# Kernel tuning notes

Hardware: AMD Instinct MI355X
Metric: run time of the kernel (lower is better)

## Reference

```python
import jax, jax.numpy as jnp
import numpy as np

BATCH, SEQ, D_MODEL, N_HEADS, D_HEAD = 2, 2048, 2048, 16, 128
ATTN_SCALE = np.sqrt(D_HEAD).astype(np.float32)
IGNORE = jnp.float32(-1e5)


def setup_inputs() -> dict:
    key = jax.random.key(0)
    ks = jax.random.split(key, 5)
    init = 1.0 / np.sqrt(D_MODEL)
    return {
        "x": jax.random.normal(ks[0], (BATCH, SEQ, D_MODEL), jnp.float32),
        "W_Q": jax.random.normal(ks[1], (N_HEADS, D_MODEL, D_HEAD), jnp.float32) * init,
        "W_K": jax.random.normal(ks[2], (N_HEADS, D_MODEL, D_HEAD), jnp.float32) * init,
        "W_V": jax.random.normal(ks[3], (N_HEADS, D_MODEL, D_HEAD), jnp.float32) * init,
        "W_O": jax.random.normal(ks[4], (N_HEADS, D_HEAD, D_MODEL), jnp.float32) * init,
        "b_Q": jnp.zeros((N_HEADS, D_HEAD), jnp.float32),
        "b_K": jnp.zeros((N_HEADS, D_HEAD), jnp.float32),
        "b_V": jnp.zeros((N_HEADS, D_HEAD), jnp.float32),
        "b_O": jnp.zeros((D_MODEL,), jnp.float32),
    }


def reference(x, W_Q, W_K, W_V, W_O, b_Q, b_K, b_V, b_O):
    # q,k,v: [batch, pos, head, d_head]
    q = jnp.einsum('bpd,hde->bphe', x, W_Q) + b_Q
    k = jnp.einsum('bpd,hde->bphe', x, W_K) + b_K
    v = jnp.einsum('bpd,hde->bphe', x, W_V) + b_V
    # scores: [batch, head, query_pos, key_pos]
    scores = jnp.einsum('bqhe,bkhe->bhqk', q, k) / ATTN_SCALE
    S = x.shape[1]
    causal = jnp.tril(jnp.ones((S, S), bool))
    scores = jnp.where(causal, scores, IGNORE)
    attn = jax.nn.softmax(scores, axis=-1)
    z = jnp.einsum('bkhe,bhqk->bqhe', v, attn)
    out = jnp.einsum('bqhe,hed->bqd', z, W_O) + b_O
    return out
```

## Files before the change

### kernel.cpp

```cpp
#include <hip/hip_runtime.h>

typedef unsigned int uint;
typedef unsigned short ushort;
typedef __bf16 bf16x8 __attribute__((ext_vector_type(8)));
typedef float f32x4 __attribute__((ext_vector_type(4)));
typedef uint u32x4 __attribute__((ext_vector_type(4)));

#define DEV static __device__ __forceinline__

#define BATCH 2
#define SEQ 2048
#define DMODEL 2048
#define NHEADS 16
#define DHEAD 128
#define MROWS (BATCH*SEQ)
#define RSCALE 0.08838834764831845f
#define LOG2E  1.4426950408889634f

DEV float fast_exp2(float x) { return __builtin_amdgcn_exp2f(x); }

DEV bf16x8 as_frag(u32x4 v) { return __builtin_bit_cast(bf16x8, v); }
DEV ushort f2bf(float f) {
  uint u = __builtin_bit_cast(uint, f);
  u += 0x7fffu + ((u >> 16) & 1u);
  return (ushort)(u >> 16);
}
DEV u32x4 lds_ld16(const ushort* p) { return *(const u32x4*)p; }

DEV void async_cp16(const ushort* g, ushort* l) {
  __builtin_amdgcn_global_load_lds(
      (const __attribute__((address_space(1))) uint*)g,
      (__attribute__((address_space(3))) uint*)l, 16, 0, 0);
}

__global__ __launch_bounds__(256) void prep(
    const float* __restrict__ x,
    const float* __restrict__ Wq, const float* __restrict__ Wk,
    const float* __restrict__ Wv, const float* __restrict__ Wo,
    ushort* __restrict__ xb, ushort* __restrict__ WqT,
    ushort* __restrict__ WkT, ushort* __restrict__ WvT,
    ushort* __restrict__ WoT)
{
  int id = blockIdx.x;
  if (id < 8192) {
    int i = id * 256 + threadIdx.x;
    float4 v = ((const float4*)x)[i];
    union { ushort u[4]; uint2 w; } o;
    o.u[0] = f2bf(v.x); o.u[1] = f2bf(v.y); o.u[2] = f2bf(v.z); o.u[3] = f2bf(v.w);
    ((uint2*)xb)[i] = o.w;
    return;
  }
  __shared__ ushort t[64][65];
  id -= 8192;
  const float* src; ushort* dst; int R, C, c0, r0;
  if (id < 3072) {
    int which = id >> 10;
    int r = id & 1023;
    int slice = r >> 6;
    int rem = r & 63;
    int tx = rem & 1, ty = rem >> 1;
    const float* S[3] = {Wq, Wk, Wv};
    ushort* D[3] = {WqT, WkT, WvT};
    src = S[which] + (size_t)slice * DMODEL * DHEAD;
    dst = D[which] + (size_t)slice * DMODEL * DHEAD;
    R = DMODEL; C = DHEAD; c0 = tx * 64; r0 = ty * 64;
  } else {
    id -= 3072;
    int tx = id & 31, ty = id >> 5;
    src = Wo; dst = WoT; R = DMODEL; C = DMODEL; c0 = tx * 64; r0 = ty * 64;
  }
  int xx = threadIdx.x & 63, yy = threadIdx.x >> 6;
  #pragma unroll
  for (int i = 0; i < 64; i += 4)
    t[yy + i][xx] = f2bf(src[(size_t)(r0 + yy + i) * C + (c0 + xx)]);
  __syncthreads();
  #pragma unroll
  for (int i = 0; i < 64; i += 4)
    dst[(size_t)(c0 + yy + i) * R + (r0 + xx)] = t[xx][yy + i];
}

__global__ __launch_bounds__(256, 4) void gemm_qkv(
    const ushort* __restrict__ xb, const ushort* __restrict__ BtAll,
    const float* __restrict__ biasAll, ushort* __restrict__ Out, int which)
{
  int mt = blockIdx.x;
  int h  = blockIdx.y;
  const ushort* Bt = BtAll + (size_t)h * DHEAD * DMODEL;
  const float* bias = biasAll + h * DHEAD;

  __shared__ __align__(16) ushort As[128 * 64];
  __shared__ __align__(16) ushort Bs[128 * 64];

  int tid = threadIdx.x, lane = tid & 63, w = tid >> 6;
  int wm = w >> 1, wn = w & 1;
  int l16 = lane & 15, quad = lane >> 4;

  const ushort* Ag = xb + (size_t)(mt * 128) * DMODEL;

  int soff[4]; int sc[4];
  #pragma unroll
  for (int t = 0; t < 4; t++) {
    int c = w * 4 + t;
    int r = c * 8 + (lane >> 3);
    int p = lane & 7;
    int g = p ^ (r & 7);
    soff[t] = r * DMODEL + g * 8;
    sc[t] = c * 512;
  }

  f32x4 acc[4][4] = {};

  for (int k0 = 0; k0 < DMODEL; k0 += 64) {
    __syncthreads();
    #pragma unroll
    for (int t = 0; t < 4; t++) {
      async_cp16(Ag + soff[t] + k0, As + sc[t]);
      async_cp16(Bt + soff[t] + k0, Bs + sc[t]);
    }
    __syncthreads();
    #pragma unroll
    for (int kk = 0; kk < 2; kk++) {
      bf16x8 a[4], b[4];
      #pragma unroll
      for (int i = 0; i < 4; i++) {
        int row = wm * 64 + i * 16 + l16;
        int p = (kk * 4 + quad) ^ (l16 & 7);
        a[i] = as_frag(lds_ld16(As + row * 64 + p * 8));
      }
      #pragma unroll
      for (int i = 0; i < 4; i++) {
        int row = wn * 64 + i * 16 + l16;
        int p = (kk * 4 + quad) ^ (l16 & 7);
        b[i] = as_frag(lds_ld16(Bs + row * 64 + p * 8));
      }
      #pragma unroll
      for (int i = 0; i < 4; i++)
        #pragma unroll
        for (int j = 0; j < 4; j++)
          acc[i][j] = __builtin_amdgcn_mfma_f32_16x16x32_bf16(a[i], b[j], acc[i][j], 0, 0, 0);
    }
  }

  float scale = (which == 0) ? RSCALE * LOG2E : 1.0f;
  #pragma unroll
  for (int i = 0; i < 4; i++) {
    #pragma unroll
    for (int j = 0; j < 4; j++) {
      int col = wn * 64 + j * 16 + l16;
      float bb = bias[col];
      #pragma unroll
      for (int r = 0; r < 4; r++) {
        int row = mt * 128 + wm * 64 + i * 16 + quad * 4 + r;
        int b_ = row >> 11, p = row & 2047;
        int bh = b_ * NHEADS + h;
        ushort val = f2bf((acc[i][j][r] + bb) * scale);
        if (which == 2) {
          Out[((size_t)bh * DHEAD + col) * SEQ + p] = val;
        } else {
          Out[((size_t)bh * SEQ + p) * DHEAD + col] = val;
        }
      }
    }
  }
}

__global__ __launch_bounds__(256, 2) void flash_attn(
    const ushort* __restrict__ Q, const ushort* __restrict__ K,
    const ushort* __restrict__ Vt, ushort* __restrict__ Z)
{
  int a  = blockIdx.x;
  int bh = blockIdx.y;
  const ushort* Qg = Q + (size_t)bh * SEQ * DHEAD;
  const ushort* Kg = K + (size_t)bh * SEQ * DHEAD;
  const ushort* Vg = Vt + (size_t)bh * DHEAD * SEQ;

  __shared__ __align__(16) ushort Ks[2][64 * 128];
  __shared__ __align__(16) ushort Vs[2][128 * 64];
  __shared__ __align__(16) ushort Ps[64 * 72];

  int tid = threadIdx.x, lane = tid & 63, w = tid >> 6;
  int l16 = lane & 15, quad = lane >> 4;

  int kOff[4], vOff[4], cLds[4];
  #pragma unroll
  for (int t = 0; t < 4; t++) {
    int c = w * 4 + t;
    cLds[t] = c * 512;
    int rk = c * 4 + (lane >> 4);
    int pk = lane & 15;
    int gk = (pk & 8) | ((pk & 7) ^ (rk & 7));
    kOff[t] = rk * DHEAD + gk * 8;
    int ev = c * 8 + (lane >> 3);
    int pv = lane & 7;
    int gv = pv ^ (ev & 7);
    vOff[t] = ev * SEQ + gv * 8;
  }

  #pragma unroll
  for (int ph = 0; ph < 2; ph++) {
    int qt = ph ? a : (31 - a);
    int q0 = qt * 64;

    bf16x8 qf[4];
    int qrow = q0 + w * 16 + l16;
    #pragma unroll
    for (int kb = 0; kb < 4; kb++)
      qf[kb] = as_frag(*(const u32x4*)(Qg + qrow * DHEAD + kb * 32 + quad * 8));

    float m_i[4], l_i[4];
    #pragma unroll
    for (int i = 0; i < 4; i++) { m_i[i] = -1e30f; l_i[i] = 0.0f; }
    f32x4 zacc[8] = {};

    #pragma unroll
    for (int t = 0; t < 4; t++) {
      async_cp16(Kg + kOff[t], Ks[0] + cLds[t]);
      async_cp16(Vg + vOff[t], Vs[0] + cLds[t]);
    }
    __syncthreads();

    for (int j = 0; j <= qt; j++) {
      int cur = j & 1;
      if (j < qt) {
        int k1 = (j + 1) * 64;
        #pragma unroll
        for (int t = 0; t < 4; t++) {
          async_cp16(Kg + k1 * DHEAD + kOff[t], Ks[cur ^ 1] + cLds[t]);
          async_cp16(Vg + k1 + vOff[t], Vs[cur ^ 1] + cLds[t]);
        }
      }
      const ushort* KsC = Ks[cur];
      const ushort* VsC = Vs[cur];

      f32x4 s[4] = {};
      #pragma unroll
      for (int kb = 0; kb < 4; kb++) {
        #pragma unroll
        for (int n = 0; n < 4; n++) {
          int r = n * 16 + l16;
          int ug = kb * 4 + quad;
          int p = (ug & 8) | ((ug & 7) ^ (r & 7));
          bf16x8 b = as_frag(lds_ld16(KsC + r * 128 + p * 8));
          s[n] = __builtin_amdgcn_mfma_f32_16x16x32_bf16(qf[kb], b, s[n], 0, 0, 0);
        }
      }
      if (j == qt) {
        #pragma unroll
        for (int n = 0; n < 4; n++)
          #pragma unroll
          for (int i = 0; i < 4; i++) {
            int qr = 16 * w + quad * 4 + i;
            int kr = n * 16 + l16;
            if (kr > qr) s[n][i] = -1e30f;
          }
      }
      float mx[4];
      #pragma unroll
      for (int i = 0; i < 4; i++)
        mx[i] = fmaxf(fmaxf(s[0][i], s[1][i]), fmaxf(s[2][i], s[3][i]));
      #pragma unroll
      for (int off = 1; off < 16; off <<= 1)
        #pragma unroll
        for (int i = 0; i < 4; i++)
          mx[i] = fmaxf(mx[i], __shfl_xor(mx[i], off, 64));

      float alpha[4], rsum[4];
      #pragma unroll
      for (int i = 0; i < 4; i++) {
        float mn = fmaxf(m_i[i], mx[i]);
        alpha[i] = fast_exp2(m_i[i] - mn);
        m_i[i] = mn;
        rsum[i] = 0.0f;
      }
      #pragma unroll
      for (int n = 0; n < 4; n++)
        #pragma unroll
        for (int i = 0; i < 4; i++) {
          float p = fast_exp2(s[n][i] - m_i[i]);
          rsum[i] += p;
          int row = 16 * w + quad * 4 + i, col = n * 16 + l16;
          Ps[row * 72 + col] = f2bf(p);
        }
      #pragma unroll
      for (int off = 1; off < 16; off <<= 1)
        #pragma unroll
        for (int i = 0; i < 4; i++)
          rsum[i] += __shfl_xor(rsum[i], off, 64);
      #pragma unroll
      for (int i = 0; i < 4; i++) l_i[i] = l_i[i] * alpha[i] + rsum[i];
      #pragma unroll
      for (int n = 0; n < 8; n++)
        #pragma unroll
        for (int i = 0; i < 4; i++) zacc[n][i] *= alpha[i];

      #pragma unroll
      for (int kk = 0; kk < 2; kk++) {
        bf16x8 af = as_frag(lds_ld16(Ps + (w * 16 + l16) * 72 + (kk * 4 + quad) * 8));
        #pragma unroll
        for (int n = 0; n < 8; n++) {
          int e = n * 16 + l16;
          int ug = kk * 4 + quad;
          int p = ug ^ (e & 7);
          bf16x8 b = as_frag(lds_ld16(VsC + e * 64 + p * 8));
          zacc[n] = __builtin_amdgcn_mfma_f32_16x16x32_bf16(af, b, zacc[n], 0, 0, 0);
        }
      }
      __syncthreads();
    }

    int b_ = bh >> 4, h = bh & 15;
    #pragma unroll
    for (int n = 0; n < 8; n++)
      #pragma unroll
      for (int i = 0; i < 4; i++) {
        int row = q0 + 16 * w + quad * 4 + i;
        int col = h * DHEAD + n * 16 + l16;
        Z[((size_t)(b_ * SEQ + row)) * DMODEL + col] = f2bf(zacc[n][i] / l_i[i]);
      }
  }
}

__global__ __launch_bounds__(256, 4) void gemm_out(
    const ushort* __restrict__ Zin, const ushort* __restrict__ WoT,
    const float* __restrict__ bO, float* __restrict__ out)
{
  int mt = blockIdx.x, ntile = blockIdx.y;
  __shared__ __align__(16) ushort As[128 * 64];
  __shared__ __align__(16) ushort Bs[128 * 64];
  int tid = threadIdx.x, lane = tid & 63, w = tid >> 6;
  int wm = w >> 1, wn = w & 1;
  int l16 = lane & 15, quad = lane >> 4;

  const ushort* Ag = Zin + (size_t)(mt * 128) * DMODEL;
  const ushort* Bg = WoT + (size_t)(ntile * 128) * DMODEL;

  int soff[4]; int sc[4];
  #pragma unroll
  for (int t = 0; t < 4; t++) {
    int c = w * 4 + t;
    int r = c * 8 + (lane >> 3);
    int p = lane & 7;
    int g = p ^ (r & 7);
    soff[t] = r * DMODEL + g * 8;
    sc[t] = c * 512;
  }

  f32x4 acc[4][4] = {};
  for (int k0 = 0; k0 < DMODEL; k0 += 64) {
    __syncthreads();
    #pragma unroll
    for (int t = 0; t < 4; t++) {
      async_cp16(Ag + soff[t] + k0, As + sc[t]);
      async_cp16(Bg + soff[t] + k0, Bs + sc[t]);
    }
    __syncthreads();
    #pragma unroll
    for (int kk = 0; kk < 2; kk++) {
      bf16x8 a[4], b[4];
      #pragma unroll
      for (int i = 0; i < 4; i++) {
        int row = wm * 64 + i * 16 + l16;
        int p = (kk * 4 + quad) ^ (l16 & 7);
        a[i] = as_frag(lds_ld16(As + row * 64 + p * 8));
      }
      #pragma unroll
      for (int i = 0; i < 4; i++) {
        int row = wn * 64 + i * 16 + l16;
        int p = (kk * 4 + quad) ^ (l16 & 7);
        b[i] = as_frag(lds_ld16(Bs + row * 64 + p * 8));
      }
      #pragma unroll
      for (int i = 0; i < 4; i++)
        #pragma unroll
        for (int j = 0; j < 4; j++)
          acc[i][j] = __builtin_amdgcn_mfma_f32_16x16x32_bf16(a[i], b[j], acc[i][j], 0, 0, 0);
    }
  }
  #pragma unroll
  for (int i = 0; i < 4; i++) {
    #pragma unroll
    for (int j = 0; j < 4; j++) {
      int col = ntile * 128 + wn * 64 + j * 16 + l16;
      float bb = bO[col];
      #pragma unroll
      for (int r = 0; r < 4; r++) {
        int row = mt * 128 + wm * 64 + i * 16 + quad * 4 + r;
        out[(size_t)row * DMODEL + col] = acc[i][j][r] + bb;
      }
    }
  }
}

extern "C" void kernel_launch(void* const* d_in, const int* in_sizes, int n_in,
                              void* d_out, int out_size, void* d_ws, size_t ws_size,
                              hipStream_t stream)
{
  const float* x  = (const float*)d_in[0];
  const float* Wq = (const float*)d_in[1];
  const float* Wk = (const float*)d_in[2];
  const float* Wv = (const float*)d_in[3];
  const float* Wo = (const float*)d_in[4];
  const float* bQ = (const float*)d_in[5];
  const float* bK = (const float*)d_in[6];
  const float* bV = (const float*)d_in[7];
  const float* bO = (const float*)d_in[8];
  float* out = (float*)d_out;

  ushort* ws = (ushort*)d_ws;
  const size_t WSZ = (size_t)NHEADS * DHEAD * DMODEL;
  const size_t QSZ = (size_t)BATCH * NHEADS * SEQ * DHEAD;
  ushort* xb  = ws;
  ushort* WqT = xb + (size_t)MROWS * DMODEL;
  ushort* WkT = WqT + WSZ;
  ushort* WvT = WkT + WSZ;
  ushort* WoT = WvT + WSZ;
  ushort* Qb  = WoT + (size_t)DMODEL * DMODEL;
  ushort* Kb  = Qb + QSZ;
  ushort* VtB = Kb + QSZ;
  ushort* Zb  = VtB + QSZ;

  dim3 tb(256);
  prep<<<dim3(12288), tb, 0, stream>>>(x, Wq, Wk, Wv, Wo,
                                       xb, WqT, WkT, WvT, WoT);

  gemm_qkv<<<dim3(32, 16), tb, 0, stream>>>(xb, WqT, bQ, Qb, 0);
  gemm_qkv<<<dim3(32, 16), tb, 0, stream>>>(xb, WkT, bK, Kb, 1);
  gemm_qkv<<<dim3(32, 16), tb, 0, stream>>>(xb, WvT, bV, VtB, 2);

  flash_attn<<<dim3(16, 32), tb, 0, stream>>>(Qb, Kb, VtB, Zb);

  gemm_out<<<dim3(32, 16), tb, 0, stream>>>(Zb, WoT, bO, out);
}
```

Measured before the change: 396.2 us.

## Merge QKV launches, single-buffer flash tiles for occupancy, remap blocks to XCDs

The three QKV projection launches become one launch, with the Q/K/V choice taken from blockIdx.z. The flash attention kernel drops its K/V double buffer and shrinks the padded P tile to a swizzled 64x64 layout, which cuts LDS use so launch bounds can rise from 2 to 4 blocks per SM. Its 2D grid is flattened and remapped so that the blocks for one batch-head group land on the same XCD, which should improve L2 reuse of K/V. The price is that global loads no longer overlap compute inside a block, and each tile needs two barriers. The design relies on higher occupancy to hide that latency instead.

New measurement: 468.5 us. 18.3% more time.

```diff
diff --git a/kernel.cpp b/kernel.cpp
--- a/kernel.cpp
+++ b/kernel.cpp
@@ -80,13 +80,20 @@
 }
 
 __global__ __launch_bounds__(256, 4) void gemm_qkv(
-    const ushort* __restrict__ xb, const ushort* __restrict__ BtAll,
-    const float* __restrict__ biasAll, ushort* __restrict__ Out, int which)
+    const ushort* __restrict__ xb,
+    const ushort* __restrict__ WqT, const ushort* __restrict__ WkT,
+    const ushort* __restrict__ WvT,
+    const float* __restrict__ bQ, const float* __restrict__ bK,
+    const float* __restrict__ bV,
+    ushort* __restrict__ Qo, ushort* __restrict__ Ko, ushort* __restrict__ Vt)
 {
   int mt = blockIdx.x;
   int h  = blockIdx.y;
-  const ushort* Bt = BtAll + (size_t)h * DHEAD * DMODEL;
-  const float* bias = biasAll + h * DHEAD;
+  int which = blockIdx.z;
+  const ushort* Bt = (which == 0) ? WqT : (which == 1) ? WkT : WvT;
+  const float* bias = (which == 0) ? bQ : (which == 1) ? bK : bV;
+  Bt += (size_t)h * DHEAD * DMODEL;
+  bias += h * DHEAD;
 
   __shared__ __align__(16) ushort As[128 * 64];
   __shared__ __align__(16) ushort Bs[128 * 64];
@@ -155,8 +162,9 @@
         int bh = b_ * NHEADS + h;
         ushort val = f2bf((acc[i][j][r] + bb) * scale);
         if (which == 2) {
-          Out[((size_t)bh * DHEAD + col) * SEQ + p] = val;
+          Vt[((size_t)bh * DHEAD + col) * SEQ + p] = val;
         } else {
+          ushort* Out = (which == 0) ? Qo : Ko;
           Out[((size_t)bh * SEQ + p) * DHEAD + col] = val;
         }
       }
@@ -164,19 +172,23 @@
   }
 }
 
-__global__ __launch_bounds__(256, 2) void flash_attn(
+__global__ __launch_bounds__(256, 4) void flash_attn(
     const ushort* __restrict__ Q, const ushort* __restrict__ K,
     const ushort* __restrict__ Vt, ushort* __restrict__ Z)
 {
-  int a  = blockIdx.x;
-  int bh = blockIdx.y;
+  int id = blockIdx.x;
+  int xcd = id & 7;
+  int j8  = id >> 3;
+  int bh  = (xcd << 2) | (j8 >> 4);
+  int a   = j8 & 15;
+
   const ushort* Qg = Q + (size_t)bh * SEQ * DHEAD;
   const ushort* Kg = K + (size_t)bh * SEQ * DHEAD;
   const ushort* Vg = Vt + (size_t)bh * DHEAD * SEQ;
 
-  __shared__ __align__(16) ushort Ks[2][64 * 128];
-  __shared__ __align__(16) ushort Vs[2][128 * 64];
-  __shared__ __align__(16) ushort Ps[64 * 72];
+  __shared__ __align__(16) ushort Ks[64 * 128];
+  __shared__ __align__(16) ushort Vs[128 * 64];
+  __shared__ __align__(16) ushort Ps[64 * 64];
 
   int tid = threadIdx.x, lane = tid & 63, w = tid >> 6;
   int l16 = lane & 15, quad = lane >> 4;
@@ -212,25 +224,15 @@
     for (int i = 0; i < 4; i++) { m_i[i] = -1e30f; l_i[i] = 0.0f; }
     f32x4 zacc[8] = {};
 
-    #pragma unroll
-    for (int t = 0; t < 4; t++) {
-      async_cp16(Kg + kOff[t], Ks[0] + cLds[t]);
-      async_cp16(Vg + vOff[t], Vs[0] + cLds[t]);
-    }
-    __syncthreads();
-
     for (int j = 0; j <= qt; j++) {
-      int cur = j & 1;
-      if (j < qt) {
-        int k1 = (j + 1) * 64;
-        #pragma unroll
-        for (int t = 0; t < 4; t++) {
-          async_cp16(Kg + k1 * DHEAD + kOff[t], Ks[cur ^ 1] + cLds[t]);
-          async_cp16(Vg + k1 + vOff[t], Vs[cur ^ 1] + cLds[t]);
-        }
-      }
-      const ushort* KsC = Ks[cur];
-      const ushort* VsC = Vs[cur];
+      int k0 = j * 64;
+      __syncthreads();
+      #pragma unroll
+      for (int t = 0; t < 4; t++) {
+        async_cp16(Kg + k0 * DHEAD + kOff[t], Ks + cLds[t]);
+        async_cp16(Vg + k0 + vOff[t], Vs + cLds[t]);
+      }
+      __syncthreads();
 
       f32x4 s[4] = {};
       #pragma unroll
@@ -240,7 +242,7 @@
           int r = n * 16 + l16;
           int ug = kb * 4 + quad;
           int p = (ug & 8) | ((ug & 7) ^ (r & 7));
-          bf16x8 b = as_frag(lds_ld16(KsC + r * 128 + p * 8));
+          bf16x8 b = as_frag(lds_ld16(Ks + r * 128 + p * 8));
           s[n] = __builtin_amdgcn_mfma_f32_16x16x32_bf16(qf[kb], b, s[n], 0, 0, 0);
         }
       }
@@ -279,7 +281,7 @@
           float p = fast_exp2(s[n][i] - m_i[i]);
           rsum[i] += p;
           int row = 16 * w + quad * 4 + i, col = n * 16 + l16;
-          Ps[row * 72 + col] = f2bf(p);
+          Ps[(row << 6) + ((((col >> 3) ^ (row & 7))) << 3) + (col & 7)] = f2bf(p);
         }
       #pragma unroll
       for (int off = 1; off < 16; off <<= 1)
@@ -295,17 +297,18 @@
 
       #pragma unroll
       for (int kk = 0; kk < 2; kk++) {
-        bf16x8 af = as_frag(lds_ld16(Ps + (w * 16 + l16) * 72 + (kk * 4 + quad) * 8));
+        int prow = w * 16 + l16;
+        int pu = (kk * 4 + quad) ^ (prow & 7);
+        bf16x8 af = as_frag(lds_ld16(Ps + (prow << 6) + (pu << 3)));
         #pragma unroll
         for (int n = 0; n < 8; n++) {
           int e = n * 16 + l16;
           int ug = kk * 4 + quad;
           int p = ug ^ (e & 7);
-          bf16x8 b = as_frag(lds_ld16(VsC + e * 64 + p * 8));
+          bf16x8 b = as_frag(lds_ld16(Vs + e * 64 + p * 8));
           zacc[n] = __builtin_amdgcn_mfma_f32_16x16x32_bf16(af, b, zacc[n], 0, 0, 0);
         }
       }
-      __syncthreads();
     }
 
     int b_ = bh >> 4, h = bh & 15;
@@ -423,11 +426,10 @@
   prep<<<dim3(12288), tb, 0, stream>>>(x, Wq, Wk, Wv, Wo,
                                        xb, WqT, WkT, WvT, WoT);
 
-  gemm_qkv<<<dim3(32, 16), tb, 0, stream>>>(xb, WqT, bQ, Qb, 0);
-  gemm_qkv<<<dim3(32, 16), tb, 0, stream>>>(xb, WkT, bK, Kb, 1);
-  gemm_qkv<<<dim3(32, 16), tb, 0, stream>>>(xb, WvT, bV, VtB, 2);
-
-  flash_attn<<<dim3(16, 32), tb, 0, stream>>>(Qb, Kb, VtB, Zb);
+  gemm_qkv<<<dim3(32, 16, 3), tb, 0, stream>>>(xb, WqT, WkT, WvT, bQ, bK, bV,
+                                               Qb, Kb, VtB);
+
+  flash_attn<<<dim3(512), tb, 0, stream>>>(Qb, Kb, VtB, Zb);
 
   gemm_out<<<dim3(32, 16), tb, 0, stream>>>(Zb, WoT, bO, out);
 }
```
